# Optimization experiments

Measured on AMD Instinct MI355X. Metric: run time of the kernel, lower is better.

## Reference

```python
import jax, jax.numpy as jnp
import numpy as np

N_NODES = 100000


def gcn_conv(x, edge_index, W, b):
    """PyG-style GCNConv: add self-loops, symmetric deg^{-1/2} normalization,
    then scatter-sum of transformed source features into targets."""
    n = x.shape[0]
    loops = jnp.arange(n, dtype=edge_index.dtype)
    row = jnp.concatenate([edge_index[0], loops])  # source
    col = jnp.concatenate([edge_index[1], loops])  # target
    deg = jax.ops.segment_sum(jnp.ones_like(col, dtype=x.dtype), col, num_segments=n)
    dinv = jnp.where(deg > 0, jax.lax.rsqrt(deg), 0.0)
    norm = dinv[row] * dinv[col]  # [E+N]
    h = x @ W  # [N, out]
    msg = h[row] * norm[:, None]  # gather + scale, [E+N, out]
    out = jax.ops.segment_sum(msg, col, num_segments=n)
    return out + b


def setup_inputs() -> dict:
    key = jax.random.key(0)
    k1, k2, k3, k4, k5 = jax.random.split(key, 5)
    x = jax.random.normal(k1, (N_NODES, 972), dtype=jnp.float32)
    edge_index = jax.random.randint(k2, (2, 1600000), 0, N_NODES, dtype=jnp.int64)
    edge_label_index = jax.random.randint(k3, (2, 1000000), 0, N_NODES, dtype=jnp.int64)
    W1 = jax.random.normal(k4, (384, 128), dtype=jnp.float32) * (1.0 / np.sqrt(384))
    b1 = jnp.zeros((128,), dtype=jnp.float32)
    W2 = jax.random.normal(k5, (128, 64), dtype=jnp.float32) * (1.0 / np.sqrt(128))
    b2 = jnp.zeros((64,), dtype=jnp.float32)
    return {"x": x, "edge_index": edge_index, "edge_label_index": edge_label_index,
            "W1": W1, "b1": b1, "W2": W2, "b2": b2}


def reference(x, edge_index, edge_label_index, W1, b1, W2, b2):
    # encode: slice features, two GCN layers with relu between
    h = x[:, 588:]  # [N, 384]
    h = jax.nn.relu(gcn_conv(h, edge_index, W1, b1))
    z = gcn_conv(h, edge_index, W2, b2)  # [N, 64]
    # decode: gather-dot-sum over labeled edges
    logits = jnp.sum(z[edge_label_index[0]] * z[edge_label_index[1]], axis=-1)
    return logits
```

## Files before the change

kernel.cpp:

```cpp
#include <hip/hip_runtime.h>
#include <hip/hip_bf16.h>

#define N_NODES 100000
#define N_EDGES 1600000
#define N_LBL   1000000
#define XC 972
#define XO 588
#define D1 128
#define D2 64
#define GEMM1_BLOCKS ((N_NODES + 63) / 64)
#define PLACE_BLOCKS (N_EDGES / 256)

typedef float f32x4 __attribute__((ext_vector_type(4)));
typedef short bf16x8 __attribute__((ext_vector_type(8)));

__device__ inline unsigned f2bf(float f) {
    unsigned u = __float_as_uint(f);
    return (u + 0x7fffu + ((u >> 16) & 1u)) >> 16;
}
__device__ inline float bf_lo(unsigned v) { return __uint_as_float(v << 16); }
__device__ inline float bf_hi(unsigned v) { return __uint_as_float(v & 0xffff0000u); }

__device__ inline unsigned pack_bf2(float lo, float hi) {
    union { __hip_bfloat162 h; unsigned u; } p;
    p.h = __float22bfloat162_rn(make_float2(lo, hi));
    return p.u;
}
__device__ inline bf16x8 to_bf8(float4 a, float4 b) {
    union { __hip_bfloat162 h[4]; bf16x8 v; } u;
    u.h[0] = __float22bfloat162_rn(make_float2(a.x, a.y));
    u.h[1] = __float22bfloat162_rn(make_float2(a.z, a.w));
    u.h[2] = __float22bfloat162_rn(make_float2(b.x, b.y));
    u.h[3] = __float22bfloat162_rn(make_float2(b.z, b.w));
    return u.v;
}
__device__ inline void add8(float (&a)[8], uint4 u) {
    a[0] += bf_lo(u.x); a[1] += bf_hi(u.x);
    a[2] += bf_lo(u.y); a[3] += bf_hi(u.y);
    a[4] += bf_lo(u.z); a[5] += bf_hi(u.z);
    a[6] += bf_lo(u.w); a[7] += bf_hi(u.w);
}
__device__ inline void fma8(float (&a)[8], uint4 u, float s) {
    a[0] = fmaf(bf_lo(u.x), s, a[0]); a[1] = fmaf(bf_hi(u.x), s, a[1]);
    a[2] = fmaf(bf_lo(u.y), s, a[2]); a[3] = fmaf(bf_hi(u.y), s, a[3]);
    a[4] = fmaf(bf_lo(u.z), s, a[4]); a[5] = fmaf(bf_hi(u.z), s, a[5]);
    a[6] = fmaf(bf_lo(u.w), s, a[6]); a[7] = fmaf(bf_hi(u.w), s, a[7]);
}

__global__ __launch_bounds__(256) void k_prep(const float* __restrict__ W1,
                                              const float* __restrict__ W2,
                                              unsigned short* __restrict__ w1p,
                                              unsigned short* __restrict__ w2p,
                                              unsigned* __restrict__ cursor) {
    int i = blockIdx.x * 256 + threadIdx.x;
    if (i < N_NODES) cursor[i] = 0u;
    if (i < 49152) {
        int j = i & 7, lane = (i >> 3) & 63, nt = (i >> 9) & 7, ks = i >> 12;
        int k = ks * 32 + ((lane >> 4) << 3) + j;
        int n = (nt << 4) + (lane & 15);
        w1p[i] = (unsigned short)f2bf(W1[k * D1 + n]);
    } else if (i < 57344) {
        int t = i - 49152;
        int j = t & 7, lane = (t >> 3) & 63, nt = (t >> 9) & 3, ks = t >> 11;
        int k = ks * 32 + ((lane >> 4) << 3) + j;
        int n = (nt << 4) + (lane & 15);
        w2p[t] = (unsigned short)f2bf(W2[k * D2 + n]);
    }
}

__global__ __launch_bounds__(256) void k_mega(const float* __restrict__ x,
                                              const unsigned short* __restrict__ w1p,
                                              unsigned short* __restrict__ s1,
                                              const int* __restrict__ erow,
                                              const int* __restrict__ ecol,
                                              unsigned* __restrict__ cursor,
                                              int* __restrict__ srcidx) {
    if (blockIdx.x < GEMM1_BLOCKS) {
        const int lane = threadIdx.x & 63;
        const int wid  = threadIdx.x >> 6;
        const int lrow = lane & 15;
        const int kq   = lane >> 4;

        const int row0 = blockIdx.x * 64 + wid * 16;
        const int rc = min(row0 + lrow, N_NODES - 1);
        const float* pA = x + (size_t)rc * XC + XO + (kq << 3);

        f32x4 acc[8];
#pragma unroll
        for (int t = 0; t < 8; ++t) acc[t] = (f32x4)0.f;

#pragma unroll 2
        for (int ks = 0; ks < 12; ++ks) {
            float4 a0 = *reinterpret_cast<const float4*>(pA + ks * 32);
            float4 a1 = *reinterpret_cast<const float4*>(pA + ks * 32 + 4);
            bf16x8 aA = to_bf8(a0, a1);
#pragma unroll
            for (int t = 0; t < 8; ++t) {
                bf16x8 bf = *reinterpret_cast<const bf16x8*>(
                    w1p + ((size_t)((ks * 8 + t) * 64 + lane) << 3));
                acc[t] = __builtin_amdgcn_mfma_f32_16x16x32_bf16(aA, bf, acc[t], 0, 0, 0);
            }
        }

        const int rowq = row0 + kq * 4;
#pragma unroll
        for (int r = 0; r < 4; ++r) {
            int rw = rowq + r;
            if (rw < N_NODES) {
#pragma unroll
                for (int t = 0; t < 8; ++t)
                    s1[(size_t)rw * D1 + lrow + t * 16] =
                        (unsigned short)f2bf(acc[t][r]);
            }
        }
    } else {
        int e = (blockIdx.x - GEMM1_BLOCKS) * 256 + threadIdx.x;
        int c = ecol[e];
        unsigned j = atomicAdd(&cursor[c], 1u);
        srcidx[((size_t)c << 6) + j] = erow[e];
    }
}

__global__ __launch_bounds__(256) void k_fused(const unsigned short* __restrict__ s1,
                                               const int* __restrict__ srcidx,
                                               const unsigned* __restrict__ deg,
                                               const float* __restrict__ b1,
                                               const unsigned short* __restrict__ w2p,
                                               unsigned short* __restrict__ s2) {
    const int lane = threadIdx.x & 63;
    const int wid  = threadIdx.x >> 6;
    const int n    = lane & 15;
    const int kq   = lane >> 4;
    const int base = blockIdx.x * 64 + wid * 16;
    const int c  = base + n;
    const int cc = min(c, N_NODES - 1);

    const int cnt = (int)deg[cc];
    const float dc = rsqrtf((float)(cnt + 1));

    float acc[4][8];
#pragma unroll
    for (int p = 0; p < 4; ++p)
#pragma unroll
        for (int j = 0; j < 8; ++j) acc[p][j] = 0.f;

    {
        const unsigned short* srow = s1 + (size_t)cc * D1 + (kq << 3);
        fma8(acc[0], *reinterpret_cast<const uint4*>(srow),      dc);
        fma8(acc[1], *reinterpret_cast<const uint4*>(srow + 32), dc);
        fma8(acc[2], *reinterpret_cast<const uint4*>(srow + 64), dc);
        fma8(acc[3], *reinterpret_cast<const uint4*>(srow + 96), dc);
    }

    const int* sp = srcidx + ((size_t)cc << 6);
    int j = 0;
    for (; j + 2 <= cnt; j += 2) {
        int2 idx = *reinterpret_cast<const int2*>(sp + j);
        float d0 = rsqrtf((float)(deg[idx.x] + 1u));
        float d1 = rsqrtf((float)(deg[idx.y] + 1u));
        const unsigned short* r0 = s1 + (size_t)idx.x * D1 + (kq << 3);
        const unsigned short* r1 = s1 + (size_t)idx.y * D1 + (kq << 3);
        uint4 a0 = *reinterpret_cast<const uint4*>(r0);
        uint4 a1 = *reinterpret_cast<const uint4*>(r0 + 32);
        uint4 a2 = *reinterpret_cast<const uint4*>(r0 + 64);
        uint4 a3 = *reinterpret_cast<const uint4*>(r0 + 96);
        uint4 c0 = *reinterpret_cast<const uint4*>(r1);
        uint4 c1 = *reinterpret_cast<const uint4*>(r1 + 32);
        uint4 c2 = *reinterpret_cast<const uint4*>(r1 + 64);
        uint4 c3 = *reinterpret_cast<const uint4*>(r1 + 96);
        fma8(acc[0], a0, d0); fma8(acc[1], a1, d0);
        fma8(acc[2], a2, d0); fma8(acc[3], a3, d0);
        fma8(acc[0], c0, d1); fma8(acc[1], c1, d1);
        fma8(acc[2], c2, d1); fma8(acc[3], c3, d1);
    }
    if (j < cnt) {
        int r = sp[j];
        float dr = rsqrtf((float)(deg[r] + 1u));
        const unsigned short* rr = s1 + (size_t)r * D1 + (kq << 3);
        fma8(acc[0], *reinterpret_cast<const uint4*>(rr),      dr);
        fma8(acc[1], *reinterpret_cast<const uint4*>(rr + 32), dr);
        fma8(acc[2], *reinterpret_cast<const uint4*>(rr + 64), dr);
        fma8(acc[3], *reinterpret_cast<const uint4*>(rr + 96), dr);
    }

    bf16x8 af[4];
#pragma unroll
    for (int p = 0; p < 4; ++p) {
        const float* bp = b1 + p * 32 + (kq << 3);
        float4 ba = *reinterpret_cast<const float4*>(bp);
        float4 bb = *reinterpret_cast<const float4*>(bp + 4);
        float4 h0 = make_float4(fmaxf(fmaf(acc[p][0], dc, ba.x), 0.f),
                                fmaxf(fmaf(acc[p][1], dc, ba.y), 0.f),
                                fmaxf(fmaf(acc[p][2], dc, ba.z), 0.f),
                                fmaxf(fmaf(acc[p][3], dc, ba.w), 0.f));
        float4 h1 = make_float4(fmaxf(fmaf(acc[p][4], dc, bb.x), 0.f),
                                fmaxf(fmaf(acc[p][5], dc, bb.y), 0.f),
                                fmaxf(fmaf(acc[p][6], dc, bb.z), 0.f),
                                fmaxf(fmaf(acc[p][7], dc, bb.w), 0.f));
        af[p] = to_bf8(h0, h1);
    }

    f32x4 acc2[4];
#pragma unroll
    for (int nt = 0; nt < 4; ++nt) acc2[nt] = (f32x4)0.f;
#pragma unroll
    for (int ks = 0; ks < 4; ++ks)
#pragma unroll
        for (int nt = 0; nt < 4; ++nt) {
            bf16x8 bf = *reinterpret_cast<const bf16x8*>(
                w2p + ((size_t)((ks * 4 + nt) * 64 + lane) << 3));
            acc2[nt] = __builtin_amdgcn_mfma_f32_16x16x32_bf16(af[ks], bf, acc2[nt], 0, 0, 0);
        }

#pragma unroll
    for (int r = 0; r < 4; ++r) {
        int rw = base + kq * 4 + r;
        if (rw < N_NODES) {
            float dm = rsqrtf((float)(deg[rw] + 1u));
#pragma unroll
            for (int nt = 0; nt < 4; ++nt)
                s2[(size_t)rw * D2 + nt * 16 + n] =
                    (unsigned short)f2bf(acc2[nt][r] * dm);
        }
    }
}

__global__ __launch_bounds__(256) void k_gather2(const unsigned short* __restrict__ s2,
                                                 const int* __restrict__ srcidx,
                                                 const unsigned* __restrict__ deg,
                                                 const float* __restrict__ b,
                                                 uint4* __restrict__ zv) {
    const int c    = blockIdx.x * 32 + (threadIdx.x >> 3);
    const int l8   = threadIdx.x & 7;

    float a[8];
#pragma unroll
    for (int j = 0; j < 8; ++j) a[j] = 0.f;
    add8(a, *reinterpret_cast<const uint4*>(s2 + (size_t)c * D2 + (l8 << 3)));

    const int cnt = (int)deg[c];
    const int* sp = srcidx + ((size_t)c << 6);
    int j = 0;
    for (; j + 4 <= cnt; j += 4) {
        int4 idx = *reinterpret_cast<const int4*>(sp + j);
        uint4 u0 = *reinterpret_cast<const uint4*>(s2 + (size_t)idx.x * D2 + (l8 << 3));
        uint4 u1 = *reinterpret_cast<const uint4*>(s2 + (size_t)idx.y * D2 + (l8 << 3));
        uint4 u2 = *reinterpret_cast<const uint4*>(s2 + (size_t)idx.z * D2 + (l8 << 3));
        uint4 u3 = *reinterpret_cast<const uint4*>(s2 + (size_t)idx.w * D2 + (l8 << 3));
        add8(a, u0); add8(a, u1); add8(a, u2); add8(a, u3);
    }
    for (; j < cnt; ++j) {
        int r = sp[j];
        add8(a, *reinterpret_cast<const uint4*>(s2 + (size_t)r * D2 + (l8 << 3)));
    }
    const float d = rsqrtf((float)(cnt + 1));
    const float4 b0 = reinterpret_cast<const float4*>(b)[l8 * 2];
    const float4 b1v = reinterpret_cast<const float4*>(b)[l8 * 2 + 1];
    uint4 o;
    o.x = pack_bf2(fmaf(a[0], d, b0.x),  fmaf(a[1], d, b0.y));
    o.y = pack_bf2(fmaf(a[2], d, b0.z),  fmaf(a[3], d, b0.w));
    o.z = pack_bf2(fmaf(a[4], d, b1v.x), fmaf(a[5], d, b1v.y));
    o.w = pack_bf2(fmaf(a[6], d, b1v.z), fmaf(a[7], d, b1v.w));
    zv[(size_t)c * 8 + l8] = o;
}

__global__ __launch_bounds__(256) void k_score(const int4* __restrict__ Z,
                                               const int* __restrict__ ea,
                                               const int* __restrict__ eb,
                                               float* __restrict__ out) {
    int tid = blockIdx.x * 256 + threadIdx.x;
    int e = tid >> 3;
    int l = tid & 7;
    int u = ea[e], v = eb[e];
    int4 a = Z[(size_t)u * 8 + l];
    int4 c = Z[(size_t)v * 8 + l];
    float p = bf_lo(a.x) * bf_lo(c.x) + bf_hi(a.x) * bf_hi(c.x)
            + bf_lo(a.y) * bf_lo(c.y) + bf_hi(a.y) * bf_hi(c.y)
            + bf_lo(a.z) * bf_lo(c.z) + bf_hi(a.z) * bf_hi(c.z)
            + bf_lo(a.w) * bf_lo(c.w) + bf_hi(a.w) * bf_hi(c.w);
    p += __shfl_down(p, 4, 8);
    p += __shfl_down(p, 2, 8);
    p += __shfl_down(p, 1, 8);
    if (l == 0) out[e] = p;
}

extern "C" void kernel_launch(void* const* d_in, const int* in_sizes, int n_in,
                              void* d_out, int out_size, void* d_ws, size_t ws_size,
                              hipStream_t stream) {
    const float* x   = (const float*)d_in[0];
    const int*   ei  = (const int*)d_in[1];
    const int*   eli = (const int*)d_in[2];
    const float* W1  = (const float*)d_in[3];
    const float* b1  = (const float*)d_in[4];
    const float* W2  = (const float*)d_in[5];
    const float* b2  = (const float*)d_in[6];
    float* out = (float*)d_out;

    char* ws = (char*)d_ws;
    unsigned*       cursor = (unsigned*)(ws + 0);
    unsigned short* w1p    = (unsigned short*)(ws + 400000);
    unsigned short* w2p    = (unsigned short*)(ws + 498304);
    int*            srcidx = (int*)(ws + 514688);
    unsigned short* s1     = (unsigned short*)(ws + 26114688);
    unsigned short* s2     = (unsigned short*)(ws + 51714688);
    unsigned short* z      = (unsigned short*)(ws + 64514688);

    k_prep   <<<392, 256, 0, stream>>>(W1, W2, w1p, w2p, cursor);
    k_mega   <<<GEMM1_BLOCKS + PLACE_BLOCKS, 256, 0, stream>>>(x, w1p, s1, ei,
                                                               ei + N_EDGES, cursor, srcidx);
    k_fused  <<<(N_NODES + 63) / 64, 256, 0, stream>>>(s1, srcidx, cursor, b1, w2p, s2);
    k_gather2<<<N_NODES / 32, 256, 0, stream>>>(s2, srcidx, cursor, b2, (uint4*)z);
    k_score  <<<(size_t)N_LBL * 8 / 256, 256, 0, stream>>>((const int4*)z, eli,
                                                           eli + N_LBL, out);
}
```

Before: 277.4 us.

## Sort nodes by degree via histogram permutation to balance gather wavefronts

```diff
diff --git a/kernel.cpp b/kernel.cpp
--- a/kernel.cpp
+++ b/kernel.cpp
@@ -51,9 +51,12 @@
                                               const float* __restrict__ W2,
                                               unsigned short* __restrict__ w1p,
                                               unsigned short* __restrict__ w2p,
-                                              unsigned* __restrict__ cursor) {
+                                              unsigned* __restrict__ cursor,
+                                              unsigned* __restrict__ ge_hist,
+                                              unsigned* __restrict__ dcur) {
     int i = blockIdx.x * 256 + threadIdx.x;
     if (i < N_NODES) cursor[i] = 0u;
+    if (i <= 64) { ge_hist[i] = (i == 0) ? (unsigned)N_NODES : 0u; dcur[i] = 0u; }
     if (i < 49152) {
         int j = i & 7, lane = (i >> 3) & 63, nt = (i >> 9) & 7, ks = i >> 12;
         int k = ks * 32 + ((lane >> 4) << 3) + j;
@@ -74,7 +77,9 @@
                                               const int* __restrict__ erow,
                                               const int* __restrict__ ecol,
                                               unsigned* __restrict__ cursor,
-                                              int* __restrict__ srcidx) {
+                                              int* __restrict__ srcidx,
+                                              unsigned* __restrict__ ge_hist) {
+    __shared__ unsigned lh[65];
     if (blockIdx.x < GEMM1_BLOCKS) {
         const int lane = threadIdx.x & 63;
         const int wid  = threadIdx.x >> 6;
@@ -114,16 +119,35 @@
             }
         }
     } else {
-        int e = (blockIdx.x - GEMM1_BLOCKS) * 256 + threadIdx.x;
+        const int tid = threadIdx.x;
+        if (tid < 65) lh[tid] = 0u;
+        __syncthreads();
+        int e = (blockIdx.x - GEMM1_BLOCKS) * 256 + tid;
         int c = ecol[e];
         unsigned j = atomicAdd(&cursor[c], 1u);
         srcidx[((size_t)c << 6) + j] = erow[e];
+        atomicAdd(&lh[min(j + 1u, 64u)], 1u);
+        __syncthreads();
+        if (tid < 65 && lh[tid]) atomicAdd(&ge_hist[tid], lh[tid]);
+    }
+}
+
+__global__ __launch_bounds__(256) void k_nplace(const unsigned* __restrict__ deg,
+                                                const unsigned* __restrict__ ge_hist,
+                                                unsigned* __restrict__ dcur,
+                                                int* __restrict__ perm) {
+    int i = blockIdx.x * 256 + threadIdx.x;
+    if (i < N_NODES) {
+        unsigned d = min(deg[i], 64u);
+        unsigned pos = (unsigned)N_NODES - ge_hist[d] + atomicAdd(&dcur[d], 1u);
+        perm[pos] = i;
     }
 }
 
 __global__ __launch_bounds__(256) void k_fused(const unsigned short* __restrict__ s1,
                                                const int* __restrict__ srcidx,
                                                const unsigned* __restrict__ deg,
+                                               const int* __restrict__ perm,
                                                const float* __restrict__ b1,
                                                const unsigned short* __restrict__ w2p,
                                                unsigned short* __restrict__ s2) {
@@ -132,10 +156,9 @@
     const int n    = lane & 15;
     const int kq   = lane >> 4;
     const int base = blockIdx.x * 64 + wid * 16;
-    const int c  = base + n;
-    const int cc = min(c, N_NODES - 1);
-
-    const int cnt = (int)deg[cc];
+    const int node = perm[min(base + n, N_NODES - 1)];
+
+    const int cnt = (int)deg[node];
     const float dc = rsqrtf((float)(cnt + 1));
 
     float acc[4][8];
@@ -145,14 +168,14 @@
         for (int j = 0; j < 8; ++j) acc[p][j] = 0.f;
 
     {
-        const unsigned short* srow = s1 + (size_t)cc * D1 + (kq << 3);
+        const unsigned short* srow = s1 + (size_t)node * D1 + (kq << 3);
         fma8(acc[0], *reinterpret_cast<const uint4*>(srow),      dc);
         fma8(acc[1], *reinterpret_cast<const uint4*>(srow + 32), dc);
         fma8(acc[2], *reinterpret_cast<const uint4*>(srow + 64), dc);
         fma8(acc[3], *reinterpret_cast<const uint4*>(srow + 96), dc);
     }
 
-    const int* sp = srcidx + ((size_t)cc << 6);
+    const int* sp = srcidx + ((size_t)node << 6);
     int j = 0;
     for (; j + 2 <= cnt; j += 2) {
         int2 idx = *reinterpret_cast<const int2*>(sp + j);
@@ -214,12 +237,13 @@
 
 #pragma unroll
     for (int r = 0; r < 4; ++r) {
-        int rw = base + kq * 4 + r;
-        if (rw < N_NODES) {
-            float dm = rsqrtf((float)(deg[rw] + 1u));
+        int slot = base + kq * 4 + r;
+        if (slot < N_NODES) {
+            int rnode = perm[slot];
+            float dm = rsqrtf((float)(deg[rnode] + 1u));
 #pragma unroll
             for (int nt = 0; nt < 4; ++nt)
-                s2[(size_t)rw * D2 + nt * 16 + n] =
+                s2[(size_t)rnode * D2 + nt * 16 + n] =
                     (unsigned short)f2bf(acc2[nt][r] * dm);
         }
     }
@@ -228,10 +252,12 @@
 __global__ __launch_bounds__(256) void k_gather2(const unsigned short* __restrict__ s2,
                                                  const int* __restrict__ srcidx,
                                                  const unsigned* __restrict__ deg,
+                                                 const int* __restrict__ perm,
                                                  const float* __restrict__ b,
                                                  uint4* __restrict__ zv) {
-    const int c    = blockIdx.x * 32 + (threadIdx.x >> 3);
+    const int slot = blockIdx.x * 32 + (threadIdx.x >> 3);
     const int l8   = threadIdx.x & 7;
+    const int c    = perm[slot];
 
     float a[8];
 #pragma unroll
@@ -297,19 +323,25 @@
     float* out = (float*)d_out;
 
     char* ws = (char*)d_ws;
-    unsigned*       cursor = (unsigned*)(ws + 0);
-    unsigned short* w1p    = (unsigned short*)(ws + 400000);
-    unsigned short* w2p    = (unsigned short*)(ws + 498304);
-    int*            srcidx = (int*)(ws + 514688);
-    unsigned short* s1     = (unsigned short*)(ws + 26114688);
-    unsigned short* s2     = (unsigned short*)(ws + 51714688);
-    unsigned short* z      = (unsigned short*)(ws + 64514688);
-
-    k_prep   <<<392, 256, 0, stream>>>(W1, W2, w1p, w2p, cursor);
+    unsigned*       cursor  = (unsigned*)(ws + 0);
+    unsigned*       ge_hist = (unsigned*)(ws + 400000);
+    unsigned*       dcur    = (unsigned*)(ws + 401024);
+    unsigned short* w1p     = (unsigned short*)(ws + 402048);
+    unsigned short* w2p     = (unsigned short*)(ws + 500352);
+    int*            perm    = (int*)(ws + 516736);
+    int*            srcidx  = (int*)(ws + 916736);
+    unsigned short* s1      = (unsigned short*)(ws + 26516736);
+    unsigned short* s2      = (unsigned short*)(ws + 52116736);
+    unsigned short* z       = (unsigned short*)(ws + 64916736);
+
+    k_prep   <<<392, 256, 0, stream>>>(W1, W2, w1p, w2p, cursor, ge_hist, dcur);
     k_mega   <<<GEMM1_BLOCKS + PLACE_BLOCKS, 256, 0, stream>>>(x, w1p, s1, ei,
-                                                               ei + N_EDGES, cursor, srcidx);
-    k_fused  <<<(N_NODES + 63) / 64, 256, 0, stream>>>(s1, srcidx, cursor, b1, w2p, s2);
-    k_gather2<<<N_NODES / 32, 256, 0, stream>>>(s2, srcidx, cursor, b2, (uint4*)z);
+                                                               ei + N_EDGES, cursor,
+                                                               srcidx, ge_hist);
+    k_nplace <<<392, 256, 0, stream>>>(cursor, ge_hist, dcur, perm);
+    k_fused  <<<(N_NODES + 63) / 64, 256, 0, stream>>>(s1, srcidx, cursor, perm, b1,
+                                                       w2p, s2);
+    k_gather2<<<N_NODES / 32, 256, 0, stream>>>(s2, srcidx, cursor, perm, b2, (uint4*)z);
     k_score  <<<(size_t)N_LBL * 8 / 256, 256, 0, stream>>>((const int4*)z, eli,
                                                            eli + N_LBL, out);
 }
```

Measured after the change: 588.9 us. 2.12x slower.
